# Performance work log

Hardware: AMD Instinct MI355X
Metric: run time of the kernel (lower is better)

## Reference

```python
import jax, jax.numpy as jnp
import numpy as np

B, S, HID = 1, 2048, 2048
H, KVH, HD = 32, 8, 64
THETA = 10000.0


def _rotate_half(x):
    x1, x2 = jnp.split(x, 2, axis=-1)
    return jnp.concatenate([-x2, x1], axis=-1)


def _rope_cos_sin(seq_len, head_dim, theta, dtype):
    inv_freq = 1.0 / (theta ** (jnp.arange(0, head_dim, 2, dtype=jnp.float32) / head_dim))
    pos = jnp.arange(seq_len, dtype=jnp.float32)
    freqs = pos[:, None] * inv_freq[None, :]          # [S, HD/2]
    emb = jnp.concatenate([freqs, freqs], axis=-1)     # [S, HD]
    return jnp.cos(emb).astype(dtype), jnp.sin(emb).astype(dtype)


def setup_inputs() -> dict:
    key = jax.random.key(0)
    k0, k1, k2, k3, k4 = jax.random.split(key, 5)
    w = lambda k, shape: jax.random.normal(k, shape, dtype=jnp.float32) * 0.02
    return {
        "hidden_states": jax.random.normal(k0, (B, S, HID), dtype=jnp.float32),
        "Wq": w(k1, (H * HD, HID)),
        "Wk": w(k2, (KVH * HD, HID)),
        "Wv": w(k3, (KVH * HD, HID)),
        "Wo": w(k4, (HID, H * HD)),
    }


def reference(hidden_states, Wq, Wk, Wv, Wo):
    b, s, _ = hidden_states.shape
    dtype = hidden_states.dtype

    # QKV projections (nn.Linear, bias=False -> x @ W.T)
    q = (hidden_states @ Wq.T).reshape(b, s, H, HD).transpose(0, 2, 1, 3)    # [b,H,s,d]
    k = (hidden_states @ Wk.T).reshape(b, s, KVH, HD).transpose(0, 2, 1, 3)  # [b,KVH,s,d]
    v = (hidden_states @ Wv.T).reshape(b, s, KVH, HD).transpose(0, 2, 1, 3)

    # RoPE (prefill: position_ids = arange(s))
    cos, sin = _rope_cos_sin(s, HD, THETA, dtype)  # [s, HD]
    apply_rope = lambda x: x * cos + _rotate_half(x) * sin
    q = apply_rope(q)
    k = apply_rope(k)

    # GQA: repeat KV heads to match query heads
    groups = H // KVH
    k = jnp.repeat(k, groups, axis=1)  # [b,H,s,d]
    v = jnp.repeat(v, groups, axis=1)

    scale = 1.0 / jnp.sqrt(jnp.asarray(HD, dtype=dtype))
    logits = jnp.einsum('bhqd,bhkd->bhqk', q, k) * scale  # [b,H,s,s]

    # prefill causal mask (phys_past_len = 0)
    causal = jnp.tril(jnp.ones((s, s), dtype=bool))
    logits = jnp.where(causal, logits, jnp.finfo(dtype).min)

    attn = jax.nn.softmax(logits, axis=-1)
    out = jnp.einsum('bhqk,bhkd->bhqd', attn, v)            # [b,H,s,d]
    out = out.transpose(0, 2, 1, 3).reshape(b, s, H * HD)   # [b,s,hidden]
    return out @ Wo.T
```

## Files before the change

### kernel.cpp

```cpp
#include <hip/hip_runtime.h>
#include <hip/hip_bf16.h>
#include <cstdint>
#include <cstddef>

#define SEQ   2048
#define HID   2048
#define NH    32
#define NKVH  8
#define HD    64
#define KVDIM (NKVH * HD)

typedef __bf16 bf16_t;
typedef __bf16 bf16x8 __attribute__((ext_vector_type(8)));
typedef float  f32x4  __attribute__((ext_vector_type(4)));

#define ROPE_L 0.4152410118609203f

#if __has_builtin(__builtin_amdgcn_exp2f)
#define QSCALE 0.18033688011112043f
#define EXPFN(x) __builtin_amdgcn_exp2f(x)
#else
#define QSCALE 0.125f
#define EXPFN(x) __expf(x)
#endif

__device__ __forceinline__ bf16x8 load8(const float* p) {
    const float4 lo = *(const float4*)p;
    const float4 hi = *(const float4*)(p + 4);
    bf16x8 r;
    r[0] = (bf16_t)lo.x; r[1] = (bf16_t)lo.y; r[2] = (bf16_t)lo.z; r[3] = (bf16_t)lo.w;
    r[4] = (bf16_t)hi.x; r[5] = (bf16_t)hi.y; r[6] = (bf16_t)hi.z; r[7] = (bf16_t)hi.w;
    return r;
}

__device__ __forceinline__ void load_lds16(const bf16_t* g, bf16_t* l) {
    __builtin_amdgcn_global_load_lds((const __attribute__((address_space(1))) void*)g,
                                     (__attribute__((address_space(3))) void*)l,
                                     16, 0, 0);
}

#define NX  (SEQ * HID)
#define NWQ (NH * HD * HID)
#define NWK (KVDIM * HID)
#define NWV (KVDIM * HID)
#define NWO (HID * NH * HD)
#define NTOT (NX + NWQ + NWK + NWV + NWO)

__global__ __launch_bounds__(256) void cvt_all(const float* __restrict__ X,
                                               const float* __restrict__ Wq,
                                               const float* __restrict__ Wk,
                                               const float* __restrict__ Wv,
                                               const float* __restrict__ Wo,
                                               bf16_t* __restrict__ Xb,
                                               bf16_t* __restrict__ Wqb,
                                               bf16_t* __restrict__ Wkb,
                                               bf16_t* __restrict__ Wvb,
                                               bf16_t* __restrict__ Wob)
{
    size_t i = ((size_t)blockIdx.x * 256 + threadIdx.x) * 8;
    if (i >= NTOT) return;
    const size_t E0 = NX, E1 = E0 + NWQ, E2 = E1 + NWK, E3 = E2 + NWV;
    const float* s; bf16_t* d; size_t off;
    if (i < E0)      { s = X;  d = Xb;  off = i; }
    else if (i < E1) { s = Wq; d = Wqb; off = i - E0; }
    else if (i < E2) { s = Wk; d = Wkb; off = i - E1; }
    else if (i < E3) { s = Wv; d = Wvb; off = i - E2; }
    else             { s = Wo; d = Wob; off = i - E3; }
    *(bf16x8*)(d + off) = load8(s + off);
}

__global__ __launch_bounds__(256) void qkv_gemm(const bf16_t* __restrict__ Xb,
                                                const bf16_t* __restrict__ Wqb,
                                                const bf16_t* __restrict__ Wkb,
                                                const bf16_t* __restrict__ Wvb,
                                                bf16_t* __restrict__ Qb,
                                                bf16_t* __restrict__ Kb,
                                                bf16_t* __restrict__ Vt)
{
    __shared__ alignas(16) bf16_t sa0[128 * 32], sa1[128 * 32];
    __shared__ alignas(16) bf16_t sb0[64 * 32],  sb1[64 * 32];
    const int t = threadIdx.x;
    const int lane = t & 63;
    const int w  = t >> 6;
    const int n16 = lane & 15;
    const int q4  = lane >> 4;
    f32x4 acc[2][4] = {};

    const int m0 = blockIdx.x * 128;
    const int n0 = blockIdx.y * 64;

    const bf16_t* B;
    int mode, nc;
    if (n0 < NH * HD)              { B = Wqb + (size_t)n0 * HID;                     mode = 0; nc = n0; }
    else if (n0 < NH * HD + KVDIM) { B = Wkb + (size_t)(n0 - NH * HD) * HID;         mode = 1; nc = n0 - NH * HD; }
    else                           { B = Wvb + (size_t)(n0 - NH * HD - KVDIM) * HID; mode = 2; nc = n0 - NH * HD - KVDIM; }

    const int lrow = lane >> 2;
    const int lcol = (lane & 3) * 8;
    const bf16_t* ag = Xb + (size_t)(m0 + w * 16 + lrow) * HID + lcol;
    const bf16_t* bg = B  + (size_t)(w * 16 + lrow) * HID + lcol;
    bf16_t* la0  = &sa0[(w * 16) * 32];
    bf16_t* la1  = &sa1[(w * 16) * 32];
    bf16_t* la0b = &sa0[(64 + w * 16) * 32];
    bf16_t* la1b = &sa1[(64 + w * 16) * 32];
    bf16_t* lb0  = &sb0[(w * 16) * 32];
    bf16_t* lb1  = &sb1[(w * 16) * 32];

    for (int k0 = 0; k0 < HID; k0 += 64) {
        load_lds16(ag + k0,                        la0);
        load_lds16(ag + k0 + 32,                   la1);
        load_lds16(ag + (size_t)64 * HID + k0,      la0b);
        load_lds16(ag + (size_t)64 * HID + k0 + 32, la1b);
        load_lds16(bg + k0,      lb0);
        load_lds16(bg + k0 + 32, lb1);
        __syncthreads();
#pragma unroll
        for (int kk = 0; kk < 2; ++kk) {
            const bf16_t* sa = kk ? sa1 : sa0;
            const bf16_t* sb = kk ? sb1 : sb0;
            bf16x8 bfrag[4];
#pragma unroll
            for (int j = 0; j < 4; ++j)
                bfrag[j] = *(const bf16x8*)&sb[(j * 16 + n16) * 32 + q4 * 8];
#pragma unroll
            for (int i = 0; i < 2; ++i) {
                bf16x8 af = *(const bf16x8*)&sa[(w * 32 + i * 16 + n16) * 32 + q4 * 8];
#pragma unroll
                for (int j = 0; j < 4; ++j)
                    acc[i][j] = __builtin_amdgcn_mfma_f32_16x16x32_bf16(af, bfrag[j], acc[i][j], 0, 0, 0);
            }
        }
        __syncthreads();
    }

    if (mode < 2) {
#pragma unroll
        for (int jt = 0; jt < 2; ++jt) {
            float dd = (float)(jt * 16 + n16);
            float inv = exp2f(-dd * ROPE_L);
#pragma unroll
            for (int i = 0; i < 2; ++i) {
#pragma unroll
                for (int r = 0; r < 4; ++r) {
                    int pos = m0 + w * 32 + i * 16 + q4 * 4 + r;
                    float ang = (float)pos * inv;
                    float sn, cs;
                    sincosf(ang, &sn, &cs);
                    float x1 = acc[i][jt][r], x2 = acc[i][jt + 2][r];
                    acc[i][jt][r]     = x1 * cs - x2 * sn;
                    acc[i][jt + 2][r] = x2 * cs + x1 * sn;
                }
            }
        }
        const float osc = (mode == 0) ? QSCALE : 1.0f;
        bf16_t* dst = (mode == 0) ? Qb : Kb;
        const int ld = (mode == 0) ? NH * HD : KVDIM;
#pragma unroll
        for (int i = 0; i < 2; ++i)
#pragma unroll
            for (int j = 0; j < 4; ++j) {
                int row = m0 + w * 32 + i * 16 + q4 * 4;
                int col = nc + j * 16 + n16;
#pragma unroll
                for (int r = 0; r < 4; ++r)
                    dst[(size_t)(row + r) * ld + col] = (bf16_t)(acc[i][j][r] * osc);
            }
    } else {
#pragma unroll
        for (int i = 0; i < 2; ++i)
#pragma unroll
            for (int j = 0; j < 4; ++j) {
                int row = m0 + w * 32 + i * 16 + q4 * 4;
                int col = nc + j * 16 + n16;
#pragma unroll
                for (int r = 0; r < 4; ++r)
                    Vt[(size_t)col * SEQ + row + r] = (bf16_t)acc[i][j][r];
            }
    }
}

__global__ __launch_bounds__(256) void o_gemm(const bf16_t* __restrict__ A,
                                              const bf16_t* __restrict__ Bw,
                                              float* __restrict__ C)
{
    __shared__ alignas(16) bf16_t sa0[128 * 32], sa1[128 * 32];
    __shared__ alignas(16) bf16_t sb0[64 * 32],  sb1[64 * 32];
    const int t = threadIdx.x;
    const int lane = t & 63;
    const int w  = t >> 6;
    const int n16 = lane & 15;
    const int q4  = lane >> 4;
    f32x4 acc[2][4] = {};

    const int m0 = blockIdx.x * 128;
    const int n0 = blockIdx.y * 64;

    const int lrow = lane >> 2;
    const int lcol = (lane & 3) * 8;
    const bf16_t* ag = A  + (size_t)(m0 + w * 16 + lrow) * HID + lcol;
    const bf16_t* bg = Bw + (size_t)(n0 + w * 16 + lrow) * HID + lcol;
    bf16_t* la0  = &sa0[(w * 16) * 32];
    bf16_t* la1  = &sa1[(w * 16) * 32];
    bf16_t* la0b = &sa0[(64 + w * 16) * 32];
    bf16_t* la1b = &sa1[(64 + w * 16) * 32];
    bf16_t* lb0  = &sb0[(w * 16) * 32];
    bf16_t* lb1  = &sb1[(w * 16) * 32];

    for (int k0 = 0; k0 < HID; k0 += 64) {
        load_lds16(ag + k0,                        la0);
        load_lds16(ag + k0 + 32,                   la1);
        load_lds16(ag + (size_t)64 * HID + k0,      la0b);
        load_lds16(ag + (size_t)64 * HID + k0 + 32, la1b);
        load_lds16(bg + k0,      lb0);
        load_lds16(bg + k0 + 32, lb1);
        __syncthreads();
#pragma unroll
        for (int kk = 0; kk < 2; ++kk) {
            const bf16_t* sa = kk ? sa1 : sa0;
            const bf16_t* sb = kk ? sb1 : sb0;
            bf16x8 bfrag[4];
#pragma unroll
            for (int j = 0; j < 4; ++j)
                bfrag[j] = *(const bf16x8*)&sb[(j * 16 + n16) * 32 + q4 * 8];
#pragma unroll
            for (int i = 0; i < 2; ++i) {
                bf16x8 af = *(const bf16x8*)&sa[(w * 32 + i * 16 + n16) * 32 + q4 * 8];
#pragma unroll
                for (int j = 0; j < 4; ++j)
                    acc[i][j] = __builtin_amdgcn_mfma_f32_16x16x32_bf16(af, bfrag[j], acc[i][j], 0, 0, 0);
            }
        }
        __syncthreads();
    }

#pragma unroll
    for (int i = 0; i < 2; ++i)
#pragma unroll
        for (int j = 0; j < 4; ++j) {
            int row = m0 + w * 32 + i * 16 + q4 * 4;
            int col = n0 + j * 16 + n16;
#pragma unroll
            for (int r = 0; r < 4; ++r)
                C[(size_t)(row + r) * HID + col] = acc[i][j][r];
        }
}

__global__ __launch_bounds__(256, 3) void attn_mfma(const bf16_t* __restrict__ Qm,
                                                    const bf16_t* __restrict__ Km,
                                                    const bf16_t* __restrict__ Vt,
                                                    bf16_t* __restrict__ Om)
{
    const int bid = blockIdx.x;
    const int h   = bid & (NH - 1);
    const int qt  = (bid < (SEQ / 128) * NH / 2)
                      ? (SEQ / 128 - 1 - (bid >> 5))
                      : ((bid - (SEQ / 128) * NH / 2) >> 5);
    const int q0  = qt * 128;
    const int kvh = h >> 2;
    const int t    = threadIdx.x;
    const int w    = t >> 6;
    const int lane = t & 63;
    const int n16  = lane & 15;
    const int q4   = lane >> 4;

    __shared__ alignas(16) bf16_t kA[128 * 32];
    __shared__ alignas(16) bf16_t kB[128 * 32];
    __shared__ alignas(16) bf16_t vc0[64 * 32], vc1[64 * 32];
    __shared__ alignas(16) bf16_t vc2[64 * 32], vc3[64 * 32];
    __shared__ alignas(16) bf16_t ps[4][2][32 * 40];

    bf16x8 qf[2][2];
#pragma unroll
    for (int i = 0; i < 2; ++i) {
        const bf16_t* qp = Qm + (size_t)(q0 + w * 32 + i * 16 + n16) * HID + h * HD;
        qf[i][0] = *(const bf16x8*)(qp + q4 * 8);
        qf[i][1] = *(const bf16x8*)(qp + 32 + q4 * 8);
    }

    f32x4 acc[2][4] = {};
    f32x4 acc_l[2] = {};
    const bf16_t one = (bf16_t)1.0f;
    const bf16x8 ones8 = {one, one, one, one, one, one, one, one};

    const int srow = lane >> 2;
    const int scol = (lane & 3) * 8;
    const bf16_t* kg = Km + (size_t)kvh * HD + scol;
    const bf16_t* vg = Vt + (size_t)(kvh * HD) * SEQ;

    const int my_last = 2 * qt + (w >> 1);
    const int wkey   = (q4 & 2) << 3;
    const int rdkey  = ((n16 >> 2) & 2) << 3;

    for (int kb = 0; kb <= qt; ++kb) {
        const int k0 = kb * 128;
        {
            const int r0 = w * 16 + srow;
            const bf16_t* kp0 = kg + (size_t)(k0 + r0) * KVDIM;
            const bf16_t* kp1 = kg + (size_t)(k0 + 64 + r0) * KVDIM;
            load_lds16(kp0,      &kA[(w * 16) * 32]);
            load_lds16(kp0 + 32, &kB[(w * 16) * 32]);
            load_lds16(kp1,      &kA[(64 + w * 16) * 32]);
            load_lds16(kp1 + 32, &kB[(64 + w * 16) * 32]);
            const bf16_t* vp = vg + (size_t)r0 * SEQ + k0 + scol;
            load_lds16(vp,      &vc0[(w * 16) * 32]);
            load_lds16(vp + 32, &vc1[(w * 16) * 32]);
            load_lds16(vp + 64, &vc2[(w * 16) * 32]);
            load_lds16(vp + 96, &vc3[(w * 16) * 32]);
        }
        __syncthreads();

        for (int hh = 0; hh < 2; ++hh) {
            const int gh = 2 * kb + hh;
            if (gh > my_last) break;
            const bf16_t* kAh = &kA[hh * 64 * 32];
            const bf16_t* kBh = &kB[hh * 64 * 32];
            const bf16_t* vAh = hh ? vc2 : vc0;
            const bf16_t* vBh = hh ? vc3 : vc1;

            f32x4 st[2][4];
#pragma unroll
            for (int jt = 0; jt < 4; ++jt) {
                bf16x8 kf0 = *(const bf16x8*)&kAh[(jt * 16 + n16) * 32 + q4 * 8];
                bf16x8 kf1 = *(const bf16x8*)&kBh[(jt * 16 + n16) * 32 + q4 * 8];
#pragma unroll
                for (int i = 0; i < 2; ++i) {
                    f32x4 s = {};
                    s = __builtin_amdgcn_mfma_f32_16x16x32_bf16(qf[i][0], kf0, s, 0, 0, 0);
                    s = __builtin_amdgcn_mfma_f32_16x16x32_bf16(qf[i][1], kf1, s, 0, 0, 0);
                    st[i][jt] = s;
                }
            }

            if (gh == my_last) {
#pragma unroll
                for (int i = 0; i < 2; ++i) {
                    int rowb = q0 + w * 32 + i * 16 + q4 * 4;
#pragma unroll
                    for (int jt = 0; jt < 4; ++jt) {
                        int colg = gh * 64 + jt * 16 + n16;
#pragma unroll
                        for (int r = 0; r < 4; ++r)
                            if (colg > rowb + r) st[i][jt][r] = -1e30f;
                    }
                }
            }

#pragma unroll
            for (int i = 0; i < 2; ++i)
#pragma unroll
                for (int jt = 0; jt < 4; ++jt)
#pragma unroll
                    for (int r = 0; r < 4; ++r)
                        st[i][jt][r] = EXPFN(st[i][jt][r]);

#pragma unroll
            for (int i = 0; i < 2; ++i)
#pragma unroll
                for (int jt = 0; jt < 4; ++jt) {
                    bf16_t* ph = ps[w][jt >> 1];
                    int rowb = i * 16 + q4 * 4;
                    int csw  = ((jt & 1) * 16 + n16) ^ wkey;
#pragma unroll
                    for (int r = 0; r < 4; ++r)
                        ph[(rowb + r) * 40 + csw] = (bf16_t)st[i][jt][r];
                }

            bf16x8 pf[2][2];
#pragma unroll
            for (int i = 0; i < 2; ++i) {
                int ra = (i * 16 + n16) * 40 + ((q4 * 8) ^ rdkey);
                pf[i][0] = *(const bf16x8*)&ps[w][0][ra];
                pf[i][1] = *(const bf16x8*)&ps[w][1][ra];
            }

#pragma unroll
            for (int i = 0; i < 2; ++i) {
                acc_l[i] = __builtin_amdgcn_mfma_f32_16x16x32_bf16(pf[i][0], ones8, acc_l[i], 0, 0, 0);
                acc_l[i] = __builtin_amdgcn_mfma_f32_16x16x32_bf16(pf[i][1], ones8, acc_l[i], 0, 0, 0);
            }

#pragma unroll
            for (int jd = 0; jd < 4; ++jd) {
                bf16x8 vf0 = *(const bf16x8*)&vAh[(jd * 16 + n16) * 32 + q4 * 8];
                bf16x8 vf1 = *(const bf16x8*)&vBh[(jd * 16 + n16) * 32 + q4 * 8];
#pragma unroll
                for (int i = 0; i < 2; ++i) {
                    acc[i][jd] = __builtin_amdgcn_mfma_f32_16x16x32_bf16(pf[i][0], vf0, acc[i][jd], 0, 0, 0);
                    acc[i][jd] = __builtin_amdgcn_mfma_f32_16x16x32_bf16(pf[i][1], vf1, acc[i][jd], 0, 0, 0);
                }
            }
        }
        __syncthreads();
    }

#pragma unroll
    for (int i = 0; i < 2; ++i) {
        float linv[4];
#pragma unroll
        for (int r = 0; r < 4; ++r) linv[r] = 1.0f / acc_l[i][r];
#pragma unroll
        for (int jd = 0; jd < 4; ++jd)
#pragma unroll
            for (int r = 0; r < 4; ++r) {
                int rowg = q0 + w * 32 + i * 16 + q4 * 4 + r;
                Om[(size_t)rowg * HID + h * HD + jd * 16 + n16] = (bf16_t)(acc[i][jd][r] * linv[r]);
            }
    }
}

extern "C" void kernel_launch(void* const* d_in, const int* in_sizes, int n_in,
                              void* d_out, int out_size, void* d_ws, size_t ws_size,
                              hipStream_t stream)
{
    const float* X  = (const float*)d_in[0];
    const float* Wq = (const float*)d_in[1];
    const float* Wk = (const float*)d_in[2];
    const float* Wv = (const float*)d_in[3];
    const float* Wo = (const float*)d_in[4];
    float* out = (float*)d_out;

    bf16_t* Xb  = (bf16_t*)d_ws;
    bf16_t* Wqb = Xb  + (size_t)NX;
    bf16_t* Wkb = Wqb + (size_t)NWQ;
    bf16_t* Wvb = Wkb + (size_t)NWK;
    bf16_t* Wob = Wvb + (size_t)NWV;
    bf16_t* Qb  = Wob + (size_t)NWO;
    bf16_t* Kb  = Qb  + (size_t)SEQ * (NH * HD);
    bf16_t* Vt  = Kb  + (size_t)SEQ * KVDIM;
    bf16_t* Ob  = Vt  + (size_t)SEQ * KVDIM;

    dim3 blk(256);

    cvt_all<<<dim3((NTOT / 8 + 255) / 256), blk, 0, stream>>>(X, Wq, Wk, Wv, Wo, Xb, Wqb, Wkb, Wvb, Wob);

    qkv_gemm<<<dim3(SEQ / 128, (NH * HD + 2 * KVDIM) / 64), blk, 0, stream>>>(Xb, Wqb, Wkb, Wvb, Qb, Kb, Vt);

    attn_mfma<<<dim3((SEQ / 128) * NH), blk, 0, stream>>>(Qb, Kb, Vt, Ob);

    o_gemm<<<dim3(SEQ / 128, HID / 64), blk, 0, stream>>>(Ob, Wob, out);
}
```

Baseline: 210.9 us.

## Double-buffer LDS tiles in GEMMs and attention to overlap loads with MFMA

Both GEMM kernels and the attention kernel now use two sets of LDS buffers, so the next K-slice (or KV block of 64) is loaded while MFMAs run on the current one. This replaces the load-sync-compute-sync pattern, hiding global-to-LDS latency. Attention also drops from 128-key to 64-key stages and raises wave priority around the MFMA sections with s_setprio. The cost is double the GEMM LDS footprint, which may lower occupancy, plus more barriers per key block in attention.

Result: faster. 201.6 us (-4.4%).

```diff
diff --git a/kernel.cpp b/kernel.cpp
--- a/kernel.cpp
+++ b/kernel.cpp
@@ -77,8 +77,10 @@
                                                 bf16_t* __restrict__ Kb,
                                                 bf16_t* __restrict__ Vt)
 {
-    __shared__ alignas(16) bf16_t sa0[128 * 32], sa1[128 * 32];
-    __shared__ alignas(16) bf16_t sb0[64 * 32],  sb1[64 * 32];
+    __shared__ alignas(16) bf16_t sA00[128 * 32], sA01[128 * 32];
+    __shared__ alignas(16) bf16_t sA10[128 * 32], sA11[128 * 32];
+    __shared__ alignas(16) bf16_t sB00[64 * 32],  sB01[64 * 32];
+    __shared__ alignas(16) bf16_t sB10[64 * 32],  sB11[64 * 32];
     const int t = threadIdx.x;
     const int lane = t & 63;
     const int w  = t >> 6;
@@ -99,37 +101,39 @@
     const int lcol = (lane & 3) * 8;
     const bf16_t* ag = Xb + (size_t)(m0 + w * 16 + lrow) * HID + lcol;
     const bf16_t* bg = B  + (size_t)(w * 16 + lrow) * HID + lcol;
-    bf16_t* la0  = &sa0[(w * 16) * 32];
-    bf16_t* la1  = &sa1[(w * 16) * 32];
-    bf16_t* la0b = &sa0[(64 + w * 16) * 32];
-    bf16_t* la1b = &sa1[(64 + w * 16) * 32];
-    bf16_t* lb0  = &sb0[(w * 16) * 32];
-    bf16_t* lb1  = &sb1[(w * 16) * 32];
-
-    for (int k0 = 0; k0 < HID; k0 += 64) {
-        load_lds16(ag + k0,                        la0);
-        load_lds16(ag + k0 + 32,                   la1);
-        load_lds16(ag + (size_t)64 * HID + k0,      la0b);
-        load_lds16(ag + (size_t)64 * HID + k0 + 32, la1b);
-        load_lds16(bg + k0,      lb0);
-        load_lds16(bg + k0 + 32, lb1);
-        __syncthreads();
-#pragma unroll
-        for (int kk = 0; kk < 2; ++kk) {
-            const bf16_t* sa = kk ? sa1 : sa0;
-            const bf16_t* sb = kk ? sb1 : sb0;
-            bf16x8 bfrag[4];
+
+    auto stage = [&](bf16_t* a0, bf16_t* a1, bf16_t* b0, bf16_t* b1, int k0) {
+        load_lds16(ag + k0,                         a0 + (w * 16) * 32);
+        load_lds16(ag + k0 + 32,                    a1 + (w * 16) * 32);
+        load_lds16(ag + (size_t)64 * HID + k0,      a0 + (64 + w * 16) * 32);
+        load_lds16(ag + (size_t)64 * HID + k0 + 32, a1 + (64 + w * 16) * 32);
+        load_lds16(bg + k0,      b0 + (w * 16) * 32);
+        load_lds16(bg + k0 + 32, b1 + (w * 16) * 32);
+    };
+    auto mma_step = [&](const bf16_t* sa, const bf16_t* sb) {
+        bf16x8 bfrag[4];
+#pragma unroll
+        for (int j = 0; j < 4; ++j)
+            bfrag[j] = *(const bf16x8*)&sb[(j * 16 + n16) * 32 + q4 * 8];
+#pragma unroll
+        for (int i = 0; i < 2; ++i) {
+            bf16x8 af = *(const bf16x8*)&sa[(w * 32 + i * 16 + n16) * 32 + q4 * 8];
 #pragma unroll
             for (int j = 0; j < 4; ++j)
-                bfrag[j] = *(const bf16x8*)&sb[(j * 16 + n16) * 32 + q4 * 8];
-#pragma unroll
-            for (int i = 0; i < 2; ++i) {
-                bf16x8 af = *(const bf16x8*)&sa[(w * 32 + i * 16 + n16) * 32 + q4 * 8];
-#pragma unroll
-                for (int j = 0; j < 4; ++j)
-                    acc[i][j] = __builtin_amdgcn_mfma_f32_16x16x32_bf16(af, bfrag[j], acc[i][j], 0, 0, 0);
-            }
-        }
+                acc[i][j] = __builtin_amdgcn_mfma_f32_16x16x32_bf16(af, bfrag[j], acc[i][j], 0, 0, 0);
+        }
+    };
+
+    stage(sA00, sA01, sB00, sB01, 0);
+    __syncthreads();
+    for (int k0 = 0; k0 < HID; k0 += 128) {
+        if (k0 + 64 < HID) stage(sA10, sA11, sB10, sB11, k0 + 64);
+        mma_step(sA00, sB00);
+        mma_step(sA01, sB01);
+        __syncthreads();
+        if (k0 + 128 < HID) stage(sA00, sA01, sB00, sB01, k0 + 128);
+        mma_step(sA10, sB10);
+        mma_step(sA11, sB11);
         __syncthreads();
     }
 
@@ -183,8 +187,10 @@
                                               const bf16_t* __restrict__ Bw,
                                               float* __restrict__ C)
 {
-    __shared__ alignas(16) bf16_t sa0[128 * 32], sa1[128 * 32];
-    __shared__ alignas(16) bf16_t sb0[64 * 32],  sb1[64 * 32];
+    __shared__ alignas(16) bf16_t sA00[128 * 32], sA01[128 * 32];
+    __shared__ alignas(16) bf16_t sA10[128 * 32], sA11[128 * 32];
+    __shared__ alignas(16) bf16_t sB00[64 * 32],  sB01[64 * 32];
+    __shared__ alignas(16) bf16_t sB10[64 * 32],  sB11[64 * 32];
     const int t = threadIdx.x;
     const int lane = t & 63;
     const int w  = t >> 6;
@@ -199,37 +205,39 @@
     const int lcol = (lane & 3) * 8;
     const bf16_t* ag = A  + (size_t)(m0 + w * 16 + lrow) * HID + lcol;
     const bf16_t* bg = Bw + (size_t)(n0 + w * 16 + lrow) * HID + lcol;
-    bf16_t* la0  = &sa0[(w * 16) * 32];
-    bf16_t* la1  = &sa1[(w * 16) * 32];
-    bf16_t* la0b = &sa0[(64 + w * 16) * 32];
-    bf16_t* la1b = &sa1[(64 + w * 16) * 32];
-    bf16_t* lb0  = &sb0[(w * 16) * 32];
-    bf16_t* lb1  = &sb1[(w * 16) * 32];
-
-    for (int k0 = 0; k0 < HID; k0 += 64) {
-        load_lds16(ag + k0,                        la0);
-        load_lds16(ag + k0 + 32,                   la1);
-        load_lds16(ag + (size_t)64 * HID + k0,      la0b);
-        load_lds16(ag + (size_t)64 * HID + k0 + 32, la1b);
-        load_lds16(bg + k0,      lb0);
-        load_lds16(bg + k0 + 32, lb1);
-        __syncthreads();
-#pragma unroll
-        for (int kk = 0; kk < 2; ++kk) {
-            const bf16_t* sa = kk ? sa1 : sa0;
-            const bf16_t* sb = kk ? sb1 : sb0;
-            bf16x8 bfrag[4];
+
+    auto stage = [&](bf16_t* a0, bf16_t* a1, bf16_t* b0, bf16_t* b1, int k0) {
+        load_lds16(ag + k0,                         a0 + (w * 16) * 32);
+        load_lds16(ag + k0 + 32,                    a1 + (w * 16) * 32);
+        load_lds16(ag + (size_t)64 * HID + k0,      a0 + (64 + w * 16) * 32);
+        load_lds16(ag + (size_t)64 * HID + k0 + 32, a1 + (64 + w * 16) * 32);
+        load_lds16(bg + k0,      b0 + (w * 16) * 32);
+        load_lds16(bg + k0 + 32, b1 + (w * 16) * 32);
+    };
+    auto mma_step = [&](const bf16_t* sa, const bf16_t* sb) {
+        bf16x8 bfrag[4];
+#pragma unroll
+        for (int j = 0; j < 4; ++j)
+            bfrag[j] = *(const bf16x8*)&sb[(j * 16 + n16) * 32 + q4 * 8];
+#pragma unroll
+        for (int i = 0; i < 2; ++i) {
+            bf16x8 af = *(const bf16x8*)&sa[(w * 32 + i * 16 + n16) * 32 + q4 * 8];
 #pragma unroll
             for (int j = 0; j < 4; ++j)
-                bfrag[j] = *(const bf16x8*)&sb[(j * 16 + n16) * 32 + q4 * 8];
-#pragma unroll
-            for (int i = 0; i < 2; ++i) {
-                bf16x8 af = *(const bf16x8*)&sa[(w * 32 + i * 16 + n16) * 32 + q4 * 8];
-#pragma unroll
-                for (int j = 0; j < 4; ++j)
-                    acc[i][j] = __builtin_amdgcn_mfma_f32_16x16x32_bf16(af, bfrag[j], acc[i][j], 0, 0, 0);
-            }
-        }
+                acc[i][j] = __builtin_amdgcn_mfma_f32_16x16x32_bf16(af, bfrag[j], acc[i][j], 0, 0, 0);
+        }
+    };
+
+    stage(sA00, sA01, sB00, sB01, 0);
+    __syncthreads();
+    for (int k0 = 0; k0 < HID; k0 += 128) {
+        if (k0 + 64 < HID) stage(sA10, sA11, sB10, sB11, k0 + 64);
+        mma_step(sA00, sB00);
+        mma_step(sA01, sB01);
+        __syncthreads();
+        if (k0 + 128 < HID) stage(sA00, sA01, sB00, sB01, k0 + 128);
+        mma_step(sA10, sB10);
+        mma_step(sA11, sB11);
         __syncthreads();
     }
 
@@ -263,10 +271,10 @@
     const int n16  = lane & 15;
     const int q4   = lane >> 4;
 
-    __shared__ alignas(16) bf16_t kA[128 * 32];
-    __shared__ alignas(16) bf16_t kB[128 * 32];
-    __shared__ alignas(16) bf16_t vc0[64 * 32], vc1[64 * 32];
-    __shared__ alignas(16) bf16_t vc2[64 * 32], vc3[64 * 32];
+    __shared__ alignas(16) bf16_t k0A[64 * 32], k0B[64 * 32];
+    __shared__ alignas(16) bf16_t k1A[64 * 32], k1B[64 * 32];
+    __shared__ alignas(16) bf16_t v0A[64 * 32], v0B[64 * 32];
+    __shared__ alignas(16) bf16_t v1A[64 * 32], v1B[64 * 32];
     __shared__ alignas(16) bf16_t ps[4][2][32 * 40];
 
     bf16x8 qf[2][2];
@@ -284,112 +292,112 @@
 
     const int srow = lane >> 2;
     const int scol = (lane & 3) * 8;
+    const int r0   = w * 16 + srow;
     const bf16_t* kg = Km + (size_t)kvh * HD + scol;
     const bf16_t* vg = Vt + (size_t)(kvh * HD) * SEQ;
 
+    const int ghmax  = 2 * qt + 1;
     const int my_last = 2 * qt + (w >> 1);
     const int wkey   = (q4 & 2) << 3;
     const int rdkey  = ((n16 >> 2) & 2) << 3;
 
-    for (int kb = 0; kb <= qt; ++kb) {
-        const int k0 = kb * 128;
-        {
-            const int r0 = w * 16 + srow;
-            const bf16_t* kp0 = kg + (size_t)(k0 + r0) * KVDIM;
-            const bf16_t* kp1 = kg + (size_t)(k0 + 64 + r0) * KVDIM;
-            load_lds16(kp0,      &kA[(w * 16) * 32]);
-            load_lds16(kp0 + 32, &kB[(w * 16) * 32]);
-            load_lds16(kp1,      &kA[(64 + w * 16) * 32]);
-            load_lds16(kp1 + 32, &kB[(64 + w * 16) * 32]);
-            const bf16_t* vp = vg + (size_t)r0 * SEQ + k0 + scol;
-            load_lds16(vp,      &vc0[(w * 16) * 32]);
-            load_lds16(vp + 32, &vc1[(w * 16) * 32]);
-            load_lds16(vp + 64, &vc2[(w * 16) * 32]);
-            load_lds16(vp + 96, &vc3[(w * 16) * 32]);
-        }
-        __syncthreads();
-
-        for (int hh = 0; hh < 2; ++hh) {
-            const int gh = 2 * kb + hh;
-            if (gh > my_last) break;
-            const bf16_t* kAh = &kA[hh * 64 * 32];
-            const bf16_t* kBh = &kB[hh * 64 * 32];
-            const bf16_t* vAh = hh ? vc2 : vc0;
-            const bf16_t* vBh = hh ? vc3 : vc1;
-
-            f32x4 st[2][4];
+    auto stage = [&](int gh, bf16_t* kA_, bf16_t* kB_, bf16_t* vA_, bf16_t* vB_) {
+        const int k0 = gh * 64;
+        const bf16_t* kp = kg + (size_t)(k0 + r0) * KVDIM;
+        load_lds16(kp,      kA_ + (w * 16) * 32);
+        load_lds16(kp + 32, kB_ + (w * 16) * 32);
+        const bf16_t* vp = vg + (size_t)r0 * SEQ + k0 + scol;
+        load_lds16(vp,      vA_ + (w * 16) * 32);
+        load_lds16(vp + 32, vB_ + (w * 16) * 32);
+    };
+
+    auto compute = [&](int gh, const bf16_t* kAh, const bf16_t* kBh,
+                       const bf16_t* vAh, const bf16_t* vBh) {
+        f32x4 st[2][4];
+        __builtin_amdgcn_s_setprio(1);
+#pragma unroll
+        for (int jt = 0; jt < 4; ++jt) {
+            bf16x8 kf0 = *(const bf16x8*)&kAh[(jt * 16 + n16) * 32 + q4 * 8];
+            bf16x8 kf1 = *(const bf16x8*)&kBh[(jt * 16 + n16) * 32 + q4 * 8];
+#pragma unroll
+            for (int i = 0; i < 2; ++i) {
+                f32x4 s = {};
+                s = __builtin_amdgcn_mfma_f32_16x16x32_bf16(qf[i][0], kf0, s, 0, 0, 0);
+                s = __builtin_amdgcn_mfma_f32_16x16x32_bf16(qf[i][1], kf1, s, 0, 0, 0);
+                st[i][jt] = s;
+            }
+        }
+        __builtin_amdgcn_s_setprio(0);
+
+        if (gh == my_last) {
+#pragma unroll
+            for (int i = 0; i < 2; ++i) {
+                int rowb = q0 + w * 32 + i * 16 + q4 * 4;
+#pragma unroll
+                for (int jt = 0; jt < 4; ++jt) {
+                    int colg = gh * 64 + jt * 16 + n16;
+#pragma unroll
+                    for (int r = 0; r < 4; ++r)
+                        if (colg > rowb + r) st[i][jt][r] = -1e30f;
+                }
+            }
+        }
+
+#pragma unroll
+        for (int i = 0; i < 2; ++i)
+#pragma unroll
+            for (int jt = 0; jt < 4; ++jt)
+#pragma unroll
+                for (int r = 0; r < 4; ++r)
+                    st[i][jt][r] = EXPFN(st[i][jt][r]);
+
+#pragma unroll
+        for (int i = 0; i < 2; ++i)
 #pragma unroll
             for (int jt = 0; jt < 4; ++jt) {
-                bf16x8 kf0 = *(const bf16x8*)&kAh[(jt * 16 + n16) * 32 + q4 * 8];
-                bf16x8 kf1 = *(const bf16x8*)&kBh[(jt * 16 + n16) * 32 + q4 * 8];
-#pragma unroll
-                for (int i = 0; i < 2; ++i) {
-                    f32x4 s = {};
-                    s = __builtin_amdgcn_mfma_f32_16x16x32_bf16(qf[i][0], kf0, s, 0, 0, 0);
-                    s = __builtin_amdgcn_mfma_f32_16x16x32_bf16(qf[i][1], kf1, s, 0, 0, 0);
-                    st[i][jt] = s;
-                }
-            }
-
-            if (gh == my_last) {
-#pragma unroll
-                for (int i = 0; i < 2; ++i) {
-                    int rowb = q0 + w * 32 + i * 16 + q4 * 4;
-#pragma unroll
-                    for (int jt = 0; jt < 4; ++jt) {
-                        int colg = gh * 64 + jt * 16 + n16;
-#pragma unroll
-                        for (int r = 0; r < 4; ++r)
-                            if (colg > rowb + r) st[i][jt][r] = -1e30f;
-                    }
-                }
-            }
-
-#pragma unroll
-            for (int i = 0; i < 2; ++i)
-#pragma unroll
-                for (int jt = 0; jt < 4; ++jt)
-#pragma unroll
-                    for (int r = 0; r < 4; ++r)
-                        st[i][jt][r] = EXPFN(st[i][jt][r]);
-
-#pragma unroll
-            for (int i = 0; i < 2; ++i)
-#pragma unroll
-                for (int jt = 0; jt < 4; ++jt) {
-                    bf16_t* ph = ps[w][jt >> 1];
-                    int rowb = i * 16 + q4 * 4;
-                    int csw  = ((jt & 1) * 16 + n16) ^ wkey;
-#pragma unroll
-                    for (int r = 0; r < 4; ++r)
-                        ph[(rowb + r) * 40 + csw] = (bf16_t)st[i][jt][r];
-                }
-
-            bf16x8 pf[2][2];
+                bf16_t* ph = ps[w][jt >> 1];
+                int rowb = i * 16 + q4 * 4;
+                int csw  = ((jt & 1) * 16 + n16) ^ wkey;
+#pragma unroll
+                for (int r = 0; r < 4; ++r)
+                    ph[(rowb + r) * 40 + csw] = (bf16_t)st[i][jt][r];
+            }
+
+        bf16x8 pf[2][2];
+#pragma unroll
+        for (int i = 0; i < 2; ++i) {
+            int ra = (i * 16 + n16) * 40 + ((q4 * 8) ^ rdkey);
+            pf[i][0] = *(const bf16x8*)&ps[w][0][ra];
+            pf[i][1] = *(const bf16x8*)&ps[w][1][ra];
+        }
+
+        __builtin_amdgcn_s_setprio(1);
+#pragma unroll
+        for (int i = 0; i < 2; ++i) {
+            acc_l[i] = __builtin_amdgcn_mfma_f32_16x16x32_bf16(pf[i][0], ones8, acc_l[i], 0, 0, 0);
+            acc_l[i] = __builtin_amdgcn_mfma_f32_16x16x32_bf16(pf[i][1], ones8, acc_l[i], 0, 0, 0);
+        }
+#pragma unroll
+        for (int jd = 0; jd < 4; ++jd) {
+            bf16x8 vf0 = *(const bf16x8*)&vAh[(jd * 16 + n16) * 32 + q4 * 8];
+            bf16x8 vf1 = *(const bf16x8*)&vBh[(jd * 16 + n16) * 32 + q4 * 8];
 #pragma unroll
             for (int i = 0; i < 2; ++i) {
-                int ra = (i * 16 + n16) * 40 + ((q4 * 8) ^ rdkey);
-                pf[i][0] = *(const bf16x8*)&ps[w][0][ra];
-                pf[i][1] = *(const bf16x8*)&ps[w][1][ra];
-            }
-
-#pragma unroll
-            for (int i = 0; i < 2; ++i) {
-                acc_l[i] = __builtin_amdgcn_mfma_f32_16x16x32_bf16(pf[i][0], ones8, acc_l[i], 0, 0, 0);
-                acc_l[i] = __builtin_amdgcn_mfma_f32_16x16x32_bf16(pf[i][1], ones8, acc_l[i], 0, 0, 0);
-            }
-
-#pragma unroll
-            for (int jd = 0; jd < 4; ++jd) {
-                bf16x8 vf0 = *(const bf16x8*)&vAh[(jd * 16 + n16) * 32 + q4 * 8];
-                bf16x8 vf1 = *(const bf16x8*)&vBh[(jd * 16 + n16) * 32 + q4 * 8];
-#pragma unroll
-                for (int i = 0; i < 2; ++i) {
-                    acc[i][jd] = __builtin_amdgcn_mfma_f32_16x16x32_bf16(pf[i][0], vf0, acc[i][jd], 0, 0, 0);
-                    acc[i][jd] = __builtin_amdgcn_mfma_f32_16x16x32_bf16(pf[i][1], vf1, acc[i][jd], 0, 0, 0);
-                }
-            }
-        }
+                acc[i][jd] = __builtin_amdgcn_mfma_f32_16x16x32_bf16(pf[i][0], vf0, acc[i][jd], 0, 0, 0);
+                acc[i][jd] = __builtin_amdgcn_mfma_f32_16x16x32_bf16(pf[i][1], vf1, acc[i][jd], 0, 0, 0);
+            }
+        }
+        __builtin_amdgcn_s_setprio(0);
+    };
+
+    stage(0, k0A, k0B, v0A, v0B);
+    __syncthreads();
+    for (int gh = 0; gh <= ghmax; gh += 2) {
+        if (gh < ghmax) stage(gh + 1, k1A, k1B, v1A, v1B);
+        if (gh <= my_last) compute(gh, k0A, k0B, v0A, v0B);
+        __syncthreads();
+        if (gh + 1 < ghmax) stage(gh + 2, k0A, k0B, v0A, v0B);
+        if (gh + 1 <= my_last) compute(gh + 1, k1A, k1B, v1A, v1B);
         __syncthreads();
     }
 
```
